# Performance work log

Measured on AMD Instinct MI355X. Metric: run time of the kernel, lower is better.

## Reference

```python
import jax, jax.numpy as jnp
import numpy as np

T = 2048          # num_tokens (flattened vLLM format)
HID = 4096        # hidden_size
H = 32            # query heads
HKV = 8           # kv heads (GQA)
G = H // HKV      # queries per kv head
D = HID // H      # head_dim = 128
W = 64            # loop_window_size (sliding window, includes current token)
THETA = 10000.0   # rope base
SCALE = D ** -0.5
NEG = -1e9


def setup_inputs() -> dict:
    key = jax.random.key(0)
    ks = jax.random.split(key, 8)
    return {
        "positions": jnp.arange(T, dtype=jnp.int32),
        "hidden_states": jax.random.normal(ks[0], (T, HID), jnp.float32),
        # loop-0 global KV cache (already RoPE'd keys, as vLLM caches them)
        "k_global": jax.random.normal(ks[1], (T, HKV, D), jnp.float32),
        "v_global": jax.random.normal(ks[2], (T, HKV, D), jnp.float32),
        "w_qkv": jax.random.normal(ks[3], ((H + 2 * HKV) * D, HID), jnp.float32) * (HID ** -0.5),
        "w_o": jax.random.normal(ks[4], (HID, H * D), jnp.float32) * ((H * D) ** -0.5),
        "w_gate": jax.random.normal(ks[5], (H, D), jnp.float32) * (D ** -0.5),
        "b_gate": jnp.zeros((H,), jnp.float32),
    }


def _rope(x, pos):
    # neox-style rotary: x [T, h, D]
    half = D // 2
    inv_freq = 1.0 / (THETA ** (jnp.arange(half, dtype=jnp.float32) / half))
    f = pos.astype(jnp.float32)[:, None] * inv_freq[None, :]   # [T, half]
    cos = jnp.cos(f)[:, None, :]
    sin = jnp.sin(f)[:, None, :]
    x1, x2 = x[..., :half], x[..., half:]
    return jnp.concatenate([x1 * cos - x2 * sin, x2 * cos + x1 * sin], axis=-1)


def reference(positions, hidden_states, k_global, v_global, w_qkv, w_o, w_gate, b_gate):
    # loop_idx > 0 path: global (loop-0 KV) + local sliding-window attention, sigmoid gate blend
    qkv = hidden_states @ w_qkv.T                               # [T, (H+2*HKV)*D]
    q, k, v = jnp.split(qkv, [H * D, H * D + HKV * D], axis=-1)
    q = _rope(q.reshape(T, H, D), positions)                    # [T, H, D]
    k = _rope(k.reshape(T, HKV, D), positions)                  # [T, HKV, D]
    v = v.reshape(T, HKV, D)
    qg = q.reshape(T, HKV, G, D)

    # --- global causal attention against loop-0 cached KV ---
    s = jnp.einsum('tghd,sgd->ghts', qg, k_global) * SCALE      # [HKV, G, T, T]
    causal = positions[:, None] >= positions[None, :]
    s = jnp.where(causal[None, None], s, NEG)
    a = jax.nn.softmax(s, axis=-1)
    out_g = jnp.einsum('ghts,sgd->tghd', a, v_global).reshape(T, H * D)

    # --- local sliding-window causal attention on current KV (banded, no T x T) ---
    t = jnp.arange(T)
    idx = t[:, None] - (W - 1) + jnp.arange(W)[None, :]          # [T, W] keys i-W+1..i
    valid = idx >= 0
    idxc = jnp.clip(idx, 0, T - 1)
    kw = k[idxc]                                                 # [T, W, HKV, D]
    vw = v[idxc]
    sl = jnp.einsum('tghd,twgd->ghtw', qg, kw) * SCALE           # [HKV, G, T, W]
    sl = jnp.where(valid[None, None], sl, NEG)
    al = jax.nn.softmax(sl, axis=-1)
    out_l = jnp.einsum('ghtw,twgd->tghd', al, vw).reshape(T, H * D)

    # --- per-head sigmoid gate (diagonal trick == per-head dot product) ---
    gate = jax.nn.sigmoid(jnp.einsum('thd,hd->th', q, w_gate) + b_gate)  # [T, H]
    gate = jnp.broadcast_to(gate[:, :, None], (T, H, D)).reshape(T, H * D)

    out = out_g * gate + out_l * (1.0 - gate)
    return out @ w_o.T                                           # [T, HID]
```

## Files before the change

kernel.cpp:

```cpp
#include <hip/hip_runtime.h>
#include <hip/hip_bf16.h>
#include <math.h>

#define T 2048
#define HID 4096
#define NH 32
#define NKV 8
#define DH 128
#define QKV_N 6144
#define SCALE_F 0.08838834764831845f
#define NEGV -1e9f

typedef unsigned short u16t;
typedef __attribute__((ext_vector_type(8))) short bf8;
typedef __attribute__((ext_vector_type(4))) float f4;

__device__ __forceinline__ float bf2f(u16t x) {
  unsigned int u = ((unsigned int)x) << 16;
  return __builtin_bit_cast(float, u);
}
__device__ __forceinline__ u16t f2bf(float f) {
  unsigned int u = __builtin_bit_cast(unsigned int, f);
  u += 0x7fffu + ((u >> 16) & 1u);
  return (u16t)(u >> 16);
}

template <int F32>
__device__ __forceinline__ bf8 load8(const void* p, size_t idx) {
  if (F32) {
    const f4* fp = (const f4*)((const float*)p + idx);
    f4 a = fp[0], b = fp[1];
    bf8 r;
    r[0] = (short)f2bf(a[0]); r[1] = (short)f2bf(a[1]);
    r[2] = (short)f2bf(a[2]); r[3] = (short)f2bf(a[3]);
    r[4] = (short)f2bf(b[0]); r[5] = (short)f2bf(b[1]);
    r[6] = (short)f2bf(b[2]); r[7] = (short)f2bf(b[3]);
    return r;
  }
  return *(const bf8*)((const u16t*)p + idx);
}

__device__ __forceinline__ void gl_lds16(const u16t* g, u16t* l) {
  __builtin_amdgcn_global_load_lds(
      (const __attribute__((address_space(1))) void*)g,
      (__attribute__((address_space(3))) void*)l, 16, 0, 0);
}

#define BARR() __builtin_amdgcn_s_barrier()
#define LGKM0() asm volatile("s_waitcnt lgkmcnt(0)" ::: "memory")
#define VM4() asm volatile("s_waitcnt vmcnt(4)" ::: "memory")
#define VM2() asm volatile("s_waitcnt vmcnt(2)" ::: "memory")
#define VM0() asm volatile("s_waitcnt vmcnt(0)" ::: "memory")

__global__ __launch_bounds__(256) void cvt_bf16(const float* __restrict__ in,
                                                u16t* __restrict__ out, int n8) {
  int i = blockIdx.x * 256 + threadIdx.x;
  if (i >= n8) return;
  const f4* fp = (const f4*)(in + (size_t)i * 8);
  f4 a = fp[0], b = fp[1];
  bf8 r;
  r[0] = (short)f2bf(a[0]); r[1] = (short)f2bf(a[1]);
  r[2] = (short)f2bf(a[2]); r[3] = (short)f2bf(a[3]);
  r[4] = (short)f2bf(b[0]); r[5] = (short)f2bf(b[1]);
  r[6] = (short)f2bf(b[2]); r[7] = (short)f2bf(b[3]);
  *(bf8*)(out + (size_t)i * 8) = r;
}


__device__ __forceinline__ void stage_ht(const u16t* __restrict__ G, int K,
                                         int k0, u16t* lds, int tid) {
#pragma unroll
  for (int i = 0; i < 2; i++) {
    int c = tid + 512 * i;
    int r = c >> 3;
    int sc = (c & 7) ^ (r & 7);
    gl_lds16(G + (size_t)r * K + k0 + sc * 8, lds + c * 8);
  }
}

template <int NF, int RS>
__device__ __forceinline__ void ld_fr(bf8 (*f)[2], const u16t* buf, int rb, int quad) {
#pragma unroll
  for (int i = 0; i < NF; i++)
#pragma unroll
    for (int kq = 0; kq < 2; kq++) {
      int r = rb + i * RS;
      int ch = (kq * 4 + quad) ^ (r & 7);
      f[i][kq] = *(const bf8*)&buf[r * 64 + ch * 8];
    }
}

template <int QA, int QB>
__device__ __forceinline__ void mfma_quad(f4 (*acc)[4], const bf8 (*af)[2],
                                          const bf8 (*bf_)[2]) {
#pragma unroll
  for (int m = 0; m < 4; m++)
#pragma unroll
    for (int n = 0; n < 2; n++)
#pragma unroll
      for (int kq = 0; kq < 2; kq++)
        acc[QA * 4 + m][QB * 2 + n] = __builtin_amdgcn_mfma_f32_16x16x32_bf16(
            af[m][kq], bf_[n][kq], acc[QA * 4 + m][QB * 2 + n], 0, 0, 0);
}

template <int OUT32>
__global__ __launch_bounds__(512, 2) void gemm256(const u16t* __restrict__ A,
                                                  const u16t* __restrict__ B,
                                                  void* __restrict__ C, int N, int K) {
  __shared__ alignas(16) u16t As[2][2][128 * 64];
  __shared__ alignas(16) u16t Bs[2][2][128 * 64];
  const int tid = threadIdx.x;
  const int wave = tid >> 6, lane = tid & 63;
  const int l15 = lane & 15, quad = lane >> 4;
  const int wm = wave >> 2, wn = wave & 3;

  unsigned nwg = gridDim.x * gridDim.y;
  unsigned lin = blockIdx.y * gridDim.x + blockIdx.x;
  lin = (lin & 7) * (nwg >> 3) + (lin >> 3);
  const int bx = lin % gridDim.x, by = lin / gridDim.x;
  const int m0 = by * 256, n0 = bx * 256;

  const u16t* A0p = A + (size_t)m0 * K;
  const u16t* A1p = A0p + (size_t)128 * K;
  const u16t* B0p = B + (size_t)n0 * K;
  const u16t* B1p = B0p + (size_t)128 * K;

  const int NT = K >> 6;

  stage_ht(A0p, K, 0, &As[0][0][0], tid);
  stage_ht(B0p, K, 0, &Bs[0][0][0], tid);
  stage_ht(B1p, K, 0, &Bs[0][1][0], tid);
  stage_ht(A1p, K, 0, &As[0][1][0], tid);

  f4 acc[8][4];
#pragma unroll
  for (int i = 0; i < 8; i++)
#pragma unroll
    for (int j = 0; j < 4; j++) acc[i][j] = (f4){0.f, 0.f, 0.f, 0.f};

  VM4();
  BARR();

  bf8 af[4][2], b0f[2][2], b1f[2][2];
  const int ra = wm * 16 + l15;
  const int rb = wn * 16 + l15;

#pragma unroll 1
  for (int t = 0; t < NT; ++t) {
    const int cur = t & 1, nxt = cur ^ 1;
    const int kn = (t + 1) << 6;
    const bool st = (t + 1) < NT;
    ld_fr<4, 32>(af, &As[cur][0][0], ra, quad);
    ld_fr<2, 64>(b0f, &Bs[cur][0][0], rb, quad);
    if (st) stage_ht(A0p, K, kn, &As[nxt][0][0], tid);
    BARR(); LGKM0();
    __builtin_amdgcn_s_setprio(1);
    mfma_quad<0, 0>(acc, af, b0f);
    __builtin_amdgcn_s_setprio(0);
    if (st) { VM4(); } else { VM2(); }
    BARR();
    ld_fr<2, 64>(b1f, &Bs[cur][1][0], rb, quad);
    if (st) stage_ht(B0p, K, kn, &Bs[nxt][0][0], tid);
    BARR(); LGKM0();
    __builtin_amdgcn_s_setprio(1);
    mfma_quad<0, 1>(acc, af, b1f);
    __builtin_amdgcn_s_setprio(0);
    if (st) { VM4(); } else { VM0(); }
    BARR();
    ld_fr<4, 32>(af, &As[cur][1][0], ra, quad);
    if (st) stage_ht(B1p, K, kn, &Bs[nxt][1][0], tid);
    BARR(); LGKM0();
    __builtin_amdgcn_s_setprio(1);
    mfma_quad<1, 1>(acc, af, b1f);
    __builtin_amdgcn_s_setprio(0);
    BARR();
    if (st) stage_ht(A1p, K, kn, &As[nxt][1][0], tid);
    BARR();
    __builtin_amdgcn_s_setprio(1);
    mfma_quad<1, 0>(acc, af, b0f);
    __builtin_amdgcn_s_setprio(0);
    if (st) { VM4(); }
    BARR();
  }

#pragma unroll
  for (int fm = 0; fm < 8; fm++)
#pragma unroll
    for (int fn = 0; fn < 4; fn++)
#pragma unroll
      for (int r = 0; r < 4; r++) {
        int row = m0 + fm * 32 + wm * 16 + quad * 4 + r;
        int col = n0 + fn * 64 + wn * 16 + l15;
        if (OUT32)
          ((float*)C)[(size_t)row * N + col] = acc[fm][fn][r];
        else
          ((u16t*)C)[(size_t)row * N + col] = f2bf(acc[fm][fn][r]);
      }
}

__global__ __launch_bounds__(256) void prep_kernel(
    const int* __restrict__ positions, const u16t* __restrict__ qkv,
    const float* __restrict__ kg_in, const float* __restrict__ wg,
    const float* __restrict__ bg, u16t* __restrict__ Qr, u16t* __restrict__ Kl,
    u16t* __restrict__ KG, float* __restrict__ gate) {
  const int t = blockIdx.x, tid = threadIdx.x;
  const float pos = (float)positions[t];
  const u16t* row = qkv + (size_t)t * QKV_N;
  float gp = 0.f;
#pragma unroll
  for (int i = 0; i < 8; i++) {
    int p = tid * 8 + i;
    int h = p >> 6, dp = p & 63;
    float invf = exp2f(-0.20762050593045702f * (float)dp);
    float f = pos * invf;
    float c = cosf(f), s = sinf(f);
    float x1 = bf2f(row[h * DH + dp]);
    float x2 = bf2f(row[h * DH + dp + 64]);
    float o1 = x1 * c - x2 * s;
    float o2 = x2 * c + x1 * s;
    Qr[(size_t)t * HID + h * DH + dp] = f2bf(o1);
    Qr[(size_t)t * HID + h * DH + dp + 64] = f2bf(o2);
    gp += o1 * wg[h * DH + dp] + o2 * wg[h * DH + dp + 64];
  }
  gp += __shfl_xor(gp, 1, 64);
  gp += __shfl_xor(gp, 2, 64);
  gp += __shfl_xor(gp, 4, 64);
  if ((tid & 7) == 0) {
    int h = tid >> 3;
    gate[t * NH + h] = 1.f / (1.f + expf(-(gp + bg[h])));
  }
  const u16t* krow = row + HID;
#pragma unroll
  for (int i = 0; i < 2; i++) {
    int p = tid * 2 + i;
    int g = p >> 6, dp = p & 63;
    float invf = exp2f(-0.20762050593045702f * (float)dp);
    float f = pos * invf;
    float c = cosf(f), s = sinf(f);
    float x1 = bf2f(krow[g * DH + dp]);
    float x2 = bf2f(krow[g * DH + dp + 64]);
    Kl[(size_t)g * T * DH + t * DH + dp] = f2bf(x1 * c - x2 * s);
    Kl[(size_t)g * T * DH + t * DH + dp + 64] = f2bf(x2 * c + x1 * s);
  }
  {
    int d4 = tid * 4;
    int g = d4 >> 7, d = d4 & 127;
    const float* src = kg_in + (size_t)t * (NKV * DH) + d4;
    u16t* dst = KG + (size_t)g * T * DH + t * DH + d;
    dst[0] = f2bf(src[0]); dst[1] = f2bf(src[1]);
    dst[2] = f2bf(src[2]); dst[3] = f2bf(src[3]);
  }
}

template <int F32>
__global__ __launch_bounds__(256) void transpose_gd(const void* __restrict__ in,
                                                    u16t* __restrict__ out,
                                                    int istride, int coff) {
  __shared__ u16t tile[64][72];
  const int g = blockIdx.z;
  const int t0 = blockIdx.x * 64, d0 = blockIdx.y * 64;
  u16t* dst = out + (size_t)g * DH * T;
  const int tid = threadIdx.x;
#pragma unroll
  for (int i = 0; i < 2; i++) {
    int c = tid + 256 * i;
    int r = c >> 3, dch = (c & 7) << 3;
    size_t idx = (size_t)coff + g * DH + (size_t)(t0 + r) * istride + d0 + dch;
    *(bf8*)&tile[r][dch] = load8<F32>(in, idx);
  }
  __syncthreads();
#pragma unroll
  for (int i = 0; i < 2; i++) {
    int c = tid + 256 * i;
    int d = c >> 3, tch = (c & 7) << 3;
    bf8 v;
#pragma unroll
    for (int j = 0; j < 8; j++) v[j] = tile[tch + j][d];
    *(bf8*)&dst[(size_t)(d0 + d) * T + t0 + tch] = v;
  }
}

template <int LOCAL>
__global__ __launch_bounds__(256) void attn_kernel(
    const u16t* __restrict__ Qr, const u16t* __restrict__ Kbase,
    const u16t* __restrict__ VTbase, const float* __restrict__ gate,
    const u16t* __restrict__ oL, u16t* __restrict__ outp) {
  __shared__ u16t k_lds[64 * 136];
  __shared__ u16t v_lds[128 * 72];
  __shared__ u16t p_lds[128 * 72];
  const int h = blockIdx.x, qt = blockIdx.y;
  const int g = h >> 2;
  const int tid = threadIdx.x, wave = tid >> 6, lane = tid & 63;
  const int l15 = lane & 15, quad = lane >> 4;
  const int q0 = qt * 128 + wave * 32;
  const u16t* K = Kbase + (size_t)g * T * DH;
  const u16t* VT = VTbase + (size_t)g * T * DH;

  bf8 qf[2][4];
#pragma unroll
  for (int mt = 0; mt < 2; mt++)
#pragma unroll
    for (int kq = 0; kq < 4; kq++)
      qf[mt][kq] = *(const bf8*)&Qr[(size_t)(q0 + mt * 16 + l15) * HID + h * DH + kq * 32 + quad * 8];

  f4 oacc[2][8];
  float m_st[2][4], l_st[2][4];
#pragma unroll
  for (int mt = 0; mt < 2; mt++) {
#pragma unroll
    for (int dt = 0; dt < 8; dt++) oacc[mt][dt] = (f4){0.f, 0.f, 0.f, 0.f};
#pragma unroll
    for (int r = 0; r < 4; r++) { m_st[mt][r] = -__builtin_inff(); l_st[mt][r] = 0.f; }
  }

  const int jend = 2 * qt + 2;
  const int jbeg = LOCAL ? (qt > 0 ? 2 * qt - 1 : 0) : 0;
  for (int j = jbeg; j < jend; j++) {
    const int kv0 = j * 64;
    __syncthreads();
#pragma unroll
    for (int i = 0; i < 4; i++) {
      int c = tid + 256 * i;
      int r = c >> 4, dch = (c & 15) << 3;
      *(bf8*)&k_lds[r * 136 + dch] = *(const bf8*)&K[(size_t)(kv0 + r) * DH + dch];
      int dd = c >> 3, kch = (c & 7) << 3;
      *(bf8*)&v_lds[dd * 72 + kch] = *(const bf8*)&VT[(size_t)dd * T + kv0 + kch];
    }
    __syncthreads();
    f4 s[2][4];
#pragma unroll
    for (int nt = 0; nt < 4; nt++) {
      bf8 kb[4];
#pragma unroll
      for (int kq = 0; kq < 4; kq++)
        kb[kq] = *(const bf8*)&k_lds[(nt * 16 + l15) * 136 + kq * 32 + quad * 8];
#pragma unroll
      for (int mt = 0; mt < 2; mt++) {
        f4 a = (f4){0.f, 0.f, 0.f, 0.f};
#pragma unroll
        for (int kq = 0; kq < 4; kq++)
          a = __builtin_amdgcn_mfma_f32_16x16x32_bf16(qf[mt][kq], kb[kq], a, 0, 0, 0);
        s[mt][nt] = a;
      }
    }
#pragma unroll
    for (int mt = 0; mt < 2; mt++)
#pragma unroll
      for (int nt = 0; nt < 4; nt++)
#pragma unroll
        for (int r = 0; r < 4; r++) {
          float v = s[mt][nt][r] * SCALE_F;
          int qq = q0 + mt * 16 + quad * 4 + r;
          int kk = kv0 + nt * 16 + l15;
          bool ok = LOCAL ? (kk <= qq && kk >= qq - 63) : (kk <= qq);
          s[mt][nt][r] = ok ? v : NEGV;
        }
    float alpha[2][4], mn[2][4], rs[2][4];
#pragma unroll
    for (int mt = 0; mt < 2; mt++)
#pragma unroll
      for (int r = 0; r < 4; r++) {
        float rm = fmaxf(fmaxf(s[mt][0][r], s[mt][1][r]), fmaxf(s[mt][2][r], s[mt][3][r]));
        rm = fmaxf(rm, __shfl_xor(rm, 1, 64));
        rm = fmaxf(rm, __shfl_xor(rm, 2, 64));
        rm = fmaxf(rm, __shfl_xor(rm, 4, 64));
        rm = fmaxf(rm, __shfl_xor(rm, 8, 64));
        float m2 = fmaxf(m_st[mt][r], rm);
        alpha[mt][r] = __expf(m_st[mt][r] - m2);
        m_st[mt][r] = m2;
        mn[mt][r] = m2;
        rs[mt][r] = 0.f;
      }
#pragma unroll
    for (int mt = 0; mt < 2; mt++)
#pragma unroll
      for (int nt = 0; nt < 4; nt++)
#pragma unroll
        for (int r = 0; r < 4; r++) {
          float p = __expf(s[mt][nt][r] - mn[mt][r]);
          rs[mt][r] += p;
          p_lds[(wave * 32 + mt * 16 + quad * 4 + r) * 72 + nt * 16 + l15] = f2bf(p);
        }
#pragma unroll
    for (int mt = 0; mt < 2; mt++)
#pragma unroll
      for (int r = 0; r < 4; r++) {
        float t0 = rs[mt][r];
        t0 += __shfl_xor(t0, 1, 64);
        t0 += __shfl_xor(t0, 2, 64);
        t0 += __shfl_xor(t0, 4, 64);
        t0 += __shfl_xor(t0, 8, 64);
        l_st[mt][r] = l_st[mt][r] * alpha[mt][r] + t0;
      }
#pragma unroll
    for (int mt = 0; mt < 2; mt++)
#pragma unroll
      for (int dt = 0; dt < 8; dt++) {
        f4 o = oacc[mt][dt];
        o[0] *= alpha[mt][0]; o[1] *= alpha[mt][1];
        o[2] *= alpha[mt][2]; o[3] *= alpha[mt][3];
        oacc[mt][dt] = o;
      }
    __syncthreads();
    bf8 pa[2][2];
#pragma unroll
    for (int mt = 0; mt < 2; mt++)
#pragma unroll
      for (int kq = 0; kq < 2; kq++)
        pa[mt][kq] = *(const bf8*)&p_lds[(wave * 32 + mt * 16 + l15) * 72 + kq * 32 + quad * 8];
#pragma unroll
    for (int dt = 0; dt < 8; dt++) {
      bf8 vb[2];
#pragma unroll
      for (int kq = 0; kq < 2; kq++)
        vb[kq] = *(const bf8*)&v_lds[(dt * 16 + l15) * 72 + kq * 32 + quad * 8];
#pragma unroll
      for (int mt = 0; mt < 2; mt++) {
        oacc[mt][dt] = __builtin_amdgcn_mfma_f32_16x16x32_bf16(pa[mt][0], vb[0], oacc[mt][dt], 0, 0, 0);
        oacc[mt][dt] = __builtin_amdgcn_mfma_f32_16x16x32_bf16(pa[mt][1], vb[1], oacc[mt][dt], 0, 0, 0);
      }
    }
  }
#pragma unroll
  for (int mt = 0; mt < 2; mt++)
#pragma unroll
    for (int r = 0; r < 4; r++) {
      int tq = q0 + mt * 16 + quad * 4 + r;
      float inv_l = 1.f / l_st[mt][r];
      if (LOCAL) {
#pragma unroll
        for (int dt = 0; dt < 8; dt++) {
          int col = dt * 16 + l15;
          outp[(size_t)tq * HID + h * DH + col] = f2bf(oacc[mt][dt][r] * inv_l);
        }
      } else {
        float gt = gate[tq * NH + h];
#pragma unroll
        for (int dt = 0; dt < 8; dt++) {
          int col = dt * 16 + l15;
          float ov = oacc[mt][dt][r] * inv_l;
          float ol = bf2f(oL[(size_t)tq * HID + h * DH + col]);
          outp[(size_t)tq * HID + h * DH + col] = f2bf(ov * gt + ol * (1.f - gt));
        }
      }
    }
}

extern "C" void kernel_launch(void* const* d_in, const int* in_sizes, int n_in,
                              void* d_out, int out_size, void* d_ws, size_t ws_size,
                              hipStream_t stream) {
  (void)in_sizes; (void)n_in; (void)out_size; (void)ws_size;
  const int* positions = (const int*)d_in[0];
  const float* hidden = (const float*)d_in[1];
  const float* k_global = (const float*)d_in[2];
  const void* v_global = d_in[3];
  const float* w_qkv = (const float*)d_in[4];
  const float* w_o = (const float*)d_in[5];
  const float* w_gate = (const float*)d_in[6];
  const float* b_gate = (const float*)d_in[7];
  float* out = (float*)d_out;

  char* ws = (char*)d_ws;
  size_t off = 0;
  u16t* qkv = (u16t*)(ws + off); off += (size_t)T * QKV_N * 2;
  u16t* Qr  = (u16t*)(ws + off); off += (size_t)T * HID * 2;
  u16t* Kl  = (u16t*)(ws + off); off += (size_t)NKV * T * DH * 2;
  u16t* KG  = (u16t*)(ws + off); off += (size_t)NKV * T * DH * 2;
  u16t* VlT = (u16t*)(ws + off); off += (size_t)NKV * T * DH * 2;
  u16t* VGT = (u16t*)(ws + off); off += (size_t)NKV * T * DH * 2;
  float* gateb = (float*)(ws + off); off += (size_t)T * NH * 4;
  u16t* out_l = (u16t*)(ws + off); off += (size_t)T * HID * 2;
  u16t* out_c = (u16t*)(ws + off); off += (size_t)T * HID * 2;
  u16t* hid_bf  = (u16t*)(ws + off);
  u16t* wqkv_bf = (u16t*)(ws + off + (size_t)T * HID * 2);
  u16t* wo_bf   = hid_bf;

  cvt_bf16<<<(T * HID / 8) / 256, 256, 0, stream>>>(hidden, hid_bf, T * HID / 8);
  cvt_bf16<<<(QKV_N * HID / 8) / 256, 256, 0, stream>>>(w_qkv, wqkv_bf, QKV_N * HID / 8);
  gemm256<0><<<dim3(QKV_N / 256, T / 256), 512, 0, stream>>>(hid_bf, wqkv_bf, qkv, QKV_N, HID);
  cvt_bf16<<<(HID * HID / 8) / 256, 256, 0, stream>>>(w_o, wo_bf, HID * HID / 8);
  prep_kernel<<<T, 256, 0, stream>>>(positions, qkv, k_global, w_gate, b_gate, Qr, Kl, KG, gateb);
  transpose_gd<0><<<dim3(T / 64, DH / 64, NKV), 256, 0, stream>>>(qkv, VlT, QKV_N, HID + NKV * DH);
  transpose_gd<1><<<dim3(T / 64, DH / 64, NKV), 256, 0, stream>>>(v_global, VGT, NKV * DH, 0);
  attn_kernel<1><<<dim3(NH, T / 128), 256, 0, stream>>>(Qr, Kl, VlT, nullptr, nullptr, out_l);
  attn_kernel<0><<<dim3(NH, T / 128), 256, 0, stream>>>(Qr, KG, VGT, gateb, out_l, out_c);
  gemm256<1><<<dim3(HID / 256, T / 256), 512, 0, stream>>>(out_c, wo_bf, out, HID, HID);
}
```

Baseline: 706.5 us.

## Stream attention K/V to swizzled LDS, reverse tile order, skip full-tile masking

Result: faster. 659.8 us (-6.6%).

```diff
diff --git a/kernel.cpp b/kernel.cpp
--- a/kernel.cpp
+++ b/kernel.cpp
@@ -65,7 +65,6 @@
   r[6] = (short)f2bf(b[2]); r[7] = (short)f2bf(b[3]);
   *(bf8*)(out + (size_t)i * 8) = r;
 }
-
 
 __device__ __forceinline__ void stage_ht(const u16t* __restrict__ G, int K,
                                          int k0, u16t* lds, int tid) {
@@ -285,10 +284,11 @@
     const u16t* __restrict__ Qr, const u16t* __restrict__ Kbase,
     const u16t* __restrict__ VTbase, const float* __restrict__ gate,
     const u16t* __restrict__ oL, u16t* __restrict__ outp) {
-  __shared__ u16t k_lds[64 * 136];
-  __shared__ u16t v_lds[128 * 72];
+  __shared__ alignas(16) u16t k_lds[64 * 128];
+  __shared__ alignas(16) u16t v_lds[128 * 64];
   __shared__ u16t p_lds[128 * 72];
-  const int h = blockIdx.x, qt = blockIdx.y;
+  const int h = blockIdx.x;
+  const int qt = gridDim.y - 1 - blockIdx.y;
   const int g = h >> 2;
   const int tid = threadIdx.x, wave = tid >> 6, lane = tid & 63;
   const int l15 = lane & 15, quad = lane >> 4;
@@ -321,19 +321,22 @@
 #pragma unroll
     for (int i = 0; i < 4; i++) {
       int c = tid + 256 * i;
-      int r = c >> 4, dch = (c & 15) << 3;
-      *(bf8*)&k_lds[r * 136 + dch] = *(const bf8*)&K[(size_t)(kv0 + r) * DH + dch];
-      int dd = c >> 3, kch = (c & 7) << 3;
-      *(bf8*)&v_lds[dd * 72 + kch] = *(const bf8*)&VT[(size_t)dd * T + kv0 + kch];
+      int rk = c >> 4, ck = c & 15;
+      gl_lds16(K + (size_t)(kv0 + rk) * DH + ((ck ^ (rk & 15)) << 3), &k_lds[c * 8]);
+      int rv = c >> 3, cv = c & 7;
+      gl_lds16(VT + (size_t)rv * T + kv0 + ((cv ^ (rv & 7)) << 3), &v_lds[c * 8]);
     }
     __syncthreads();
     f4 s[2][4];
+    __builtin_amdgcn_s_setprio(1);
 #pragma unroll
     for (int nt = 0; nt < 4; nt++) {
       bf8 kb[4];
 #pragma unroll
-      for (int kq = 0; kq < 4; kq++)
-        kb[kq] = *(const bf8*)&k_lds[(nt * 16 + l15) * 136 + kq * 32 + quad * 8];
+      for (int kq = 0; kq < 4; kq++) {
+        int rr = nt * 16 + l15;
+        kb[kq] = *(const bf8*)&k_lds[rr * 128 + (((kq * 4 + quad) ^ (rr & 15)) << 3)];
+      }
 #pragma unroll
       for (int mt = 0; mt < 2; mt++) {
         f4 a = (f4){0.f, 0.f, 0.f, 0.f};
@@ -343,18 +346,29 @@
         s[mt][nt] = a;
       }
     }
-#pragma unroll
-    for (int mt = 0; mt < 2; mt++)
-#pragma unroll
-      for (int nt = 0; nt < 4; nt++)
-#pragma unroll
-        for (int r = 0; r < 4; r++) {
-          float v = s[mt][nt][r] * SCALE_F;
-          int qq = q0 + mt * 16 + quad * 4 + r;
-          int kk = kv0 + nt * 16 + l15;
-          bool ok = LOCAL ? (kk <= qq && kk >= qq - 63) : (kk <= qq);
-          s[mt][nt][r] = ok ? v : NEGV;
-        }
+    __builtin_amdgcn_s_setprio(0);
+    const bool full = LOCAL ? false : (kv0 + 63 <= q0);
+    if (full) {
+#pragma unroll
+      for (int mt = 0; mt < 2; mt++)
+#pragma unroll
+        for (int nt = 0; nt < 4; nt++)
+#pragma unroll
+          for (int r = 0; r < 4; r++) s[mt][nt][r] *= SCALE_F;
+    } else {
+#pragma unroll
+      for (int mt = 0; mt < 2; mt++)
+#pragma unroll
+        for (int nt = 0; nt < 4; nt++)
+#pragma unroll
+          for (int r = 0; r < 4; r++) {
+            float v = s[mt][nt][r] * SCALE_F;
+            int qq = q0 + mt * 16 + quad * 4 + r;
+            int kk = kv0 + nt * 16 + l15;
+            bool ok = LOCAL ? (kk <= qq && kk >= qq - 63) : (kk <= qq);
+            s[mt][nt][r] = ok ? v : NEGV;
+          }
+    }
     float alpha[2][4], mn[2][4], rs[2][4];
 #pragma unroll
     for (int mt = 0; mt < 2; mt++)
@@ -401,25 +415,28 @@
         o[2] *= alpha[mt][2]; o[3] *= alpha[mt][3];
         oacc[mt][dt] = o;
       }
-    __syncthreads();
     bf8 pa[2][2];
 #pragma unroll
     for (int mt = 0; mt < 2; mt++)
 #pragma unroll
       for (int kq = 0; kq < 2; kq++)
         pa[mt][kq] = *(const bf8*)&p_lds[(wave * 32 + mt * 16 + l15) * 72 + kq * 32 + quad * 8];
+    __builtin_amdgcn_s_setprio(1);
 #pragma unroll
     for (int dt = 0; dt < 8; dt++) {
       bf8 vb[2];
 #pragma unroll
-      for (int kq = 0; kq < 2; kq++)
-        vb[kq] = *(const bf8*)&v_lds[(dt * 16 + l15) * 72 + kq * 32 + quad * 8];
+      for (int kq = 0; kq < 2; kq++) {
+        int rr = dt * 16 + l15;
+        vb[kq] = *(const bf8*)&v_lds[rr * 64 + (((kq * 4 + quad) ^ (rr & 7)) << 3)];
+      }
 #pragma unroll
       for (int mt = 0; mt < 2; mt++) {
         oacc[mt][dt] = __builtin_amdgcn_mfma_f32_16x16x32_bf16(pa[mt][0], vb[0], oacc[mt][dt], 0, 0, 0);
         oacc[mt][dt] = __builtin_amdgcn_mfma_f32_16x16x32_bf16(pa[mt][1], vb[1], oacc[mt][dt], 0, 0, 0);
       }
     }
+    __builtin_amdgcn_s_setprio(0);
   }
 #pragma unroll
   for (int mt = 0; mt < 2; mt++)
```
